# Kernel tuning notes

Hardware: AMD Instinct MI355X
Metric: run time of the kernel (lower is better)

Reference implementation:

```python
import jax, jax.numpy as jnp
import numpy as np

N = 50000
D = 128
E = 600000

def setup_inputs() -> dict:
    key = jax.random.key(0)
    k1, k2, k3, k4, k5 = jax.random.split(key, 5)
    z1 = jax.random.normal(k1, (N, D), dtype=jnp.float32)
    z2 = jax.random.normal(k2, (N, D), dtype=jnp.float32)
    adj_row = jax.random.randint(k3, (E,), 0, N, dtype=jnp.int32)
    adj_col = jax.random.randint(k4, (E,), 0, N, dtype=jnp.int32)
    adj_val = jax.random.uniform(k5, (E,), dtype=jnp.float32)
    a = jnp.full((N, D), 0.5, dtype=jnp.float32)
    b = jnp.full((N, D), 0.5, dtype=jnp.float32)
    alpha = jnp.float32(0.5)
    return {"z1": z1, "z2": z2, "adj_row": adj_row, "adj_col": adj_col,
            "adj_val": adj_val, "a": a, "b": b, "alpha": alpha}

def reference(z1, z2, adj_row, adj_col, adj_val, a, b, alpha):
    # elementwise gated combine: z_i = a*z1 + b*z2   [N, D]
    z_i = a * z1 + b * z2
    # sparse matmul: z_l[r] = sum_e adj_val[e] * z_i[adj_col[e]] for adj_row[e]==r
    msgs = adj_val[:, None] * z_i[adj_col]          # [E, D]
    z_l = jax.ops.segment_sum(msgs, adj_row, num_segments=N)  # [N, D]
    # residual blend
    return alpha * z_l + (1.0 - alpha) * z_i
```

## Files before the change

### kernel.cpp

```cpp
#include <hip/hip_runtime.h>
#include <hip/hip_fp16.h>

#define DDIM 128
#define CAPMAX 32

__global__ void __launch_bounds__(256) build_kernel(
    const float4* __restrict__ z1, const float4* __restrict__ z2,
    const float4* __restrict__ a,  const float4* __restrict__ b,
    uint2* __restrict__ zi16, int n4,
    const int* __restrict__ rows, const int* __restrict__ cols,
    const float* __restrict__ vals,
    unsigned* __restrict__ slots, int* __restrict__ cnt,
    int* __restrict__ ohead, int* __restrict__ onext,
    int cap, int E) {
  if (blockIdx.x & 1) {
    const int t = (int)(blockIdx.x >> 1) * blockDim.x + threadIdx.x;
    const int stride = (int)(gridDim.x >> 1) * blockDim.x;
    for (int e0 = t; e0 < E; e0 += 2 * stride) {
      const int e1 = e0 + stride;
      const bool has1 = e1 < E;
      const int   r0 = rows[e0];
      const int   c0 = cols[e0];
      const float v0 = vals[e0];
      const int   r1 = has1 ? rows[e1] : 0;
      const int   c1 = has1 ? cols[e1] : 0;
      const float v1 = has1 ? vals[e1] : 0.f;
      const int j0 = atomicAdd(&cnt[r0], 1);
      const int j1 = has1 ? atomicAdd(&cnt[r1], 1) : 0;
      if (j0 < cap) {
        const unsigned hv = (unsigned)__half_as_ushort(__float2half_rn(v0));
        slots[(size_t)r0 * cap + j0] = (unsigned)c0 | (hv << 16);
      } else {
        onext[e0] = atomicExch(&ohead[r0], e0 + 1);
      }
      if (has1) {
        if (j1 < cap) {
          const unsigned hv = (unsigned)__half_as_ushort(__float2half_rn(v1));
          slots[(size_t)r1 * cap + j1] = (unsigned)c1 | (hv << 16);
        } else {
          onext[e1] = atomicExch(&ohead[r1], e1 + 1);
        }
      }
    }
  } else {
    const int t = (int)(blockIdx.x >> 1) * blockDim.x + threadIdx.x;
    const int stride = (int)(gridDim.x >> 1) * blockDim.x;
    for (int j = t; j < n4; j += stride) {
      float4 A = a[j], B = b[j], X = z1[j], Y = z2[j];
      __half2 h0 = __floats2half2_rn(A.x * X.x + B.x * Y.x,
                                     A.y * X.y + B.y * Y.y);
      __half2 h1 = __floats2half2_rn(A.z * X.z + B.z * Y.z,
                                     A.w * X.w + B.w * Y.w);
      uint2 pk;
      pk.x = *reinterpret_cast<unsigned*>(&h0);
      pk.y = *reinterpret_cast<unsigned*>(&h1);
      zi16[j] = pk;
    }
  }
}

__global__ void __launch_bounds__(256) reduce_kernel(
    const unsigned* __restrict__ slots, const int* __restrict__ cnt,
    const int* __restrict__ ohead, const int* __restrict__ onext,
    const int* __restrict__ cols, const float* __restrict__ vals,
    const float* __restrict__ alpha_p,
    const __half2* __restrict__ zi16, float2* __restrict__ out2,
    int cap, int N) {
  const int r = (int)((blockIdx.x * blockDim.x + threadIdx.x) >> 6);
  const int lane = threadIdx.x & 63;
  if (r >= N) return;
  const float alpha = alpha_p[0];

  const __half2 zr16 = zi16[(size_t)r * (DDIM / 2) + lane];

  const int deg = cnt[r];
  const int m = deg < cap ? deg : cap;
  const unsigned* sp = slots + (size_t)r * cap;
  const uint4* sp4 = (const uint4*)sp;

  float2 a0 = make_float2(0.f, 0.f), a1 = a0, a2 = a0, a3 = a0;
  float2 a4 = a0, a5 = a0, a6 = a0, a7 = a0;
  int j = 0;
  for (; j + 8 <= m; j += 8) {
    const uint4 p0 = sp4[(j >> 2) + 0];
    const uint4 p1 = sp4[(j >> 2) + 1];
    const __half2 g0 = zi16[(size_t)(p0.x & 0xFFFF) * (DDIM / 2) + lane];
    const __half2 g1 = zi16[(size_t)(p0.y & 0xFFFF) * (DDIM / 2) + lane];
    const __half2 g2 = zi16[(size_t)(p0.z & 0xFFFF) * (DDIM / 2) + lane];
    const __half2 g3 = zi16[(size_t)(p0.w & 0xFFFF) * (DDIM / 2) + lane];
    const __half2 g4 = zi16[(size_t)(p1.x & 0xFFFF) * (DDIM / 2) + lane];
    const __half2 g5 = zi16[(size_t)(p1.y & 0xFFFF) * (DDIM / 2) + lane];
    const __half2 g6 = zi16[(size_t)(p1.z & 0xFFFF) * (DDIM / 2) + lane];
    const __half2 g7 = zi16[(size_t)(p1.w & 0xFFFF) * (DDIM / 2) + lane];
    const float2 f0 = __half22float2(g0), f1 = __half22float2(g1);
    const float2 f2 = __half22float2(g2), f3 = __half22float2(g3);
    const float2 f4 = __half22float2(g4), f5 = __half22float2(g5);
    const float2 f6 = __half22float2(g6), f7 = __half22float2(g7);
    const float v0 = __half2float(__ushort_as_half((unsigned short)(p0.x >> 16)));
    const float v1 = __half2float(__ushort_as_half((unsigned short)(p0.y >> 16)));
    const float v2 = __half2float(__ushort_as_half((unsigned short)(p0.z >> 16)));
    const float v3 = __half2float(__ushort_as_half((unsigned short)(p0.w >> 16)));
    const float v4 = __half2float(__ushort_as_half((unsigned short)(p1.x >> 16)));
    const float v5 = __half2float(__ushort_as_half((unsigned short)(p1.y >> 16)));
    const float v6 = __half2float(__ushort_as_half((unsigned short)(p1.z >> 16)));
    const float v7 = __half2float(__ushort_as_half((unsigned short)(p1.w >> 16)));
    a0.x += v0 * f0.x; a0.y += v0 * f0.y;
    a1.x += v1 * f1.x; a1.y += v1 * f1.y;
    a2.x += v2 * f2.x; a2.y += v2 * f2.y;
    a3.x += v3 * f3.x; a3.y += v3 * f3.y;
    a4.x += v4 * f4.x; a4.y += v4 * f4.y;
    a5.x += v5 * f5.x; a5.y += v5 * f5.y;
    a6.x += v6 * f6.x; a6.y += v6 * f6.y;
    a7.x += v7 * f7.x; a7.y += v7 * f7.y;
  }
  for (; j < m; ++j) {
    const unsigned s = sp[j];
    const float v = __half2float(__ushort_as_half((unsigned short)(s >> 16)));
    const float2 f =
        __half22float2(zi16[(size_t)(s & 0xFFFF) * (DDIM / 2) + lane]);
    a0.x += v * f.x; a0.y += v * f.y;
  }
  if (deg > cap) {
    int e1 = ohead[r];
    while (e1 > 0) {
      const int e = e1 - 1;
      e1 = onext[e];
      const int c = cols[e];
      const float v = vals[e];
      const float2 f = __half22float2(zi16[(size_t)c * (DDIM / 2) + lane]);
      a0.x += v * f.x; a0.y += v * f.y;
    }
  }

  float2 acc;
  acc.x = ((a0.x + a1.x) + (a2.x + a3.x)) + ((a4.x + a5.x) + (a6.x + a7.x));
  acc.y = ((a0.y + a1.y) + (a2.y + a3.y)) + ((a4.y + a5.y) + (a6.y + a7.y));
  const float2 zr = __half22float2(zr16);
  const float om = 1.0f - alpha;
  float2 o;
  o.x = alpha * acc.x + om * zr.x;
  o.y = alpha * acc.y + om * zr.y;
  out2[(size_t)r * (DDIM / 2) + lane] = o;
}

extern "C" void kernel_launch(void* const* d_in, const int* in_sizes, int n_in,
                              void* d_out, int out_size, void* d_ws, size_t ws_size,
                              hipStream_t stream) {
  const float* z1    = (const float*)d_in[0];
  const float* z2    = (const float*)d_in[1];
  const int*   rows  = (const int*)  d_in[2];
  const int*   cols  = (const int*)  d_in[3];
  const float* vals  = (const float*)d_in[4];
  const float* a     = (const float*)d_in[5];
  const float* b     = (const float*)d_in[6];
  const float* alpha = (const float*)d_in[7];
  float* out = (float*)d_out;

  const int ND = in_sizes[0];
  const int E  = in_sizes[2];
  const int N  = ND / DDIM;
  const int n4 = ND / 4;

  __half2* zi16 = (__half2*)d_ws;
  int* cnt   = (int*)((char*)d_ws + (size_t)ND * 2);
  int* ohead = cnt + N;
  int* onext = ohead + N;
  unsigned* slots = (unsigned*)(onext + E);

  const size_t fixed_bytes = (size_t)ND * 2 + ((size_t)2 * N + E) * 4;
  size_t avail = ws_size > fixed_bytes ? ws_size - fixed_bytes : 0;
  int cap = (int)(avail / ((size_t)N * sizeof(unsigned)));
  if (cap > CAPMAX) cap = CAPMAX;
  cap &= ~3;
  if (cap < 4) cap = 0;

  hipMemsetAsync(cnt, 0x00, (size_t)2 * N * sizeof(int), stream);

  build_kernel<<<2048, 256, 0, stream>>>(
      (const float4*)z1, (const float4*)z2, (const float4*)a,
      (const float4*)b, (uint2*)zi16, n4,
      rows, cols, vals, slots, cnt, ohead, onext, cap, E);

  const int blocks2 = (int)(((long long)N * 64 + 255) / 256);
  reduce_kernel<<<blocks2, 256, 0, stream>>>(
      slots, cnt, ohead, onext, cols, vals, alpha,
      zi16, (float2*)out, cap, N);
}
```

Measured before the change: 192.0 us.

## Split edge bucketing into eight per-partition slot arrays with separate counters

Edge bucketing now uses eight partitions, chosen by block index. Each partition has its own per-row counters and slot arrays, aiming to spread atomic contention on the row counters. The build kernel no longer splits blocks between the combine and the bucketing; every thread does the fp16 combine first and then processes edges. The reduce kernel reads all eight partition counters and the first uint4 of each partition's slots, then runs unrolled predicated gathers. In exchange it adds counter and slot traffic, a larger memset, and extra branching per row, when the average degree is already small.

```diff
diff --git a/kernel.cpp b/kernel.cpp
--- a/kernel.cpp
+++ b/kernel.cpp
@@ -2,7 +2,8 @@
 #include <hip/hip_fp16.h>
 
 #define DDIM 128
-#define CAPMAX 32
+#define NPART 8
+#define CAP8MAX 16
 
 __global__ void __launch_bounds__(256) build_kernel(
     const float4* __restrict__ z1, const float4* __restrict__ z2,
@@ -10,62 +11,62 @@
     uint2* __restrict__ zi16, int n4,
     const int* __restrict__ rows, const int* __restrict__ cols,
     const float* __restrict__ vals,
-    unsigned* __restrict__ slots, int* __restrict__ cnt,
+    unsigned* __restrict__ slots, int* __restrict__ cnt8,
     int* __restrict__ ohead, int* __restrict__ onext,
-    int cap, int E) {
-  if (blockIdx.x & 1) {
-    const int t = (int)(blockIdx.x >> 1) * blockDim.x + threadIdx.x;
-    const int stride = (int)(gridDim.x >> 1) * blockDim.x;
-    for (int e0 = t; e0 < E; e0 += 2 * stride) {
-      const int e1 = e0 + stride;
-      const bool has1 = e1 < E;
-      const int   r0 = rows[e0];
-      const int   c0 = cols[e0];
-      const float v0 = vals[e0];
-      const int   r1 = has1 ? rows[e1] : 0;
-      const int   c1 = has1 ? cols[e1] : 0;
-      const float v1 = has1 ? vals[e1] : 0.f;
-      const int j0 = atomicAdd(&cnt[r0], 1);
-      const int j1 = has1 ? atomicAdd(&cnt[r1], 1) : 0;
-      if (j0 < cap) {
-        const unsigned hv = (unsigned)__half_as_ushort(__float2half_rn(v0));
-        slots[(size_t)r0 * cap + j0] = (unsigned)c0 | (hv << 16);
+    int cap8, int N, int E) {
+  const int t = (int)blockIdx.x * (int)blockDim.x + threadIdx.x;
+  const int stride = (int)gridDim.x * (int)blockDim.x;
+
+  for (int j = t; j < n4; j += stride) {
+    float4 A = a[j], B = b[j], X = z1[j], Y = z2[j];
+    __half2 h0 = __floats2half2_rn(A.x * X.x + B.x * Y.x,
+                                   A.y * X.y + B.y * Y.y);
+    __half2 h1 = __floats2half2_rn(A.z * X.z + B.z * Y.z,
+                                   A.w * X.w + B.w * Y.w);
+    uint2 pk;
+    pk.x = *reinterpret_cast<unsigned*>(&h0);
+    pk.y = *reinterpret_cast<unsigned*>(&h1);
+    zi16[j] = pk;
+  }
+
+  const int p = (int)blockIdx.x & (NPART - 1);
+  int* __restrict__ mycnt = cnt8 + (size_t)p * N;
+  unsigned* __restrict__ myslots = slots + (size_t)p * N * cap8;
+  for (int e0 = t; e0 < E; e0 += 2 * stride) {
+    const int e1 = e0 + stride;
+    const bool has1 = e1 < E;
+    const int   r0 = rows[e0];
+    const int   c0 = cols[e0];
+    const float v0 = vals[e0];
+    const int   r1 = has1 ? rows[e1] : 0;
+    const int   c1 = has1 ? cols[e1] : 0;
+    const float v1 = has1 ? vals[e1] : 0.f;
+    const int j0 = atomicAdd(&mycnt[r0], 1);
+    const int j1 = has1 ? atomicAdd(&mycnt[r1], 1) : 0;
+    if (j0 < cap8) {
+      const unsigned hv = (unsigned)__half_as_ushort(__float2half_rn(v0));
+      myslots[(size_t)r0 * cap8 + j0] = (unsigned)c0 | (hv << 16);
+    } else {
+      onext[e0] = atomicExch(&ohead[r0], e0 + 1);
+    }
+    if (has1) {
+      if (j1 < cap8) {
+        const unsigned hv = (unsigned)__half_as_ushort(__float2half_rn(v1));
+        myslots[(size_t)r1 * cap8 + j1] = (unsigned)c1 | (hv << 16);
       } else {
-        onext[e0] = atomicExch(&ohead[r0], e0 + 1);
+        onext[e1] = atomicExch(&ohead[r1], e1 + 1);
       }
-      if (has1) {
-        if (j1 < cap) {
-          const unsigned hv = (unsigned)__half_as_ushort(__float2half_rn(v1));
-          slots[(size_t)r1 * cap + j1] = (unsigned)c1 | (hv << 16);
-        } else {
-          onext[e1] = atomicExch(&ohead[r1], e1 + 1);
-        }
-      }
-    }
-  } else {
-    const int t = (int)(blockIdx.x >> 1) * blockDim.x + threadIdx.x;
-    const int stride = (int)(gridDim.x >> 1) * blockDim.x;
-    for (int j = t; j < n4; j += stride) {
-      float4 A = a[j], B = b[j], X = z1[j], Y = z2[j];
-      __half2 h0 = __floats2half2_rn(A.x * X.x + B.x * Y.x,
-                                     A.y * X.y + B.y * Y.y);
-      __half2 h1 = __floats2half2_rn(A.z * X.z + B.z * Y.z,
-                                     A.w * X.w + B.w * Y.w);
-      uint2 pk;
-      pk.x = *reinterpret_cast<unsigned*>(&h0);
-      pk.y = *reinterpret_cast<unsigned*>(&h1);
-      zi16[j] = pk;
     }
   }
 }
 
 __global__ void __launch_bounds__(256) reduce_kernel(
-    const unsigned* __restrict__ slots, const int* __restrict__ cnt,
+    const unsigned* __restrict__ slots, const int* __restrict__ cnt8,
     const int* __restrict__ ohead, const int* __restrict__ onext,
     const int* __restrict__ cols, const float* __restrict__ vals,
     const float* __restrict__ alpha_p,
     const __half2* __restrict__ zi16, float2* __restrict__ out2,
-    int cap, int N) {
+    int cap8, int N) {
   const int r = (int)((blockIdx.x * blockDim.x + threadIdx.x) >> 6);
   const int lane = threadIdx.x & 63;
   if (r >= N) return;
@@ -73,68 +74,54 @@
 
   const __half2 zr16 = zi16[(size_t)r * (DDIM / 2) + lane];
 
-  const int deg = cnt[r];
-  const int m = deg < cap ? deg : cap;
-  const unsigned* sp = slots + (size_t)r * cap;
-  const uint4* sp4 = (const uint4*)sp;
+  int mp[NPART];
+  uint4 q[NPART];
+  bool over = false;
+#pragma unroll
+  for (int p = 0; p < NPART; ++p) {
+    const int dp = cnt8[(size_t)p * N + r];
+    mp[p] = dp < cap8 ? dp : cap8;
+    over = over || (dp > cap8);
+    q[p] = *(const uint4*)(slots + ((size_t)p * N + r) * cap8);
+  }
 
   float2 a0 = make_float2(0.f, 0.f), a1 = a0, a2 = a0, a3 = a0;
-  float2 a4 = a0, a5 = a0, a6 = a0, a7 = a0;
-  int j = 0;
-  for (; j + 8 <= m; j += 8) {
-    const uint4 p0 = sp4[(j >> 2) + 0];
-    const uint4 p1 = sp4[(j >> 2) + 1];
-    const __half2 g0 = zi16[(size_t)(p0.x & 0xFFFF) * (DDIM / 2) + lane];
-    const __half2 g1 = zi16[(size_t)(p0.y & 0xFFFF) * (DDIM / 2) + lane];
-    const __half2 g2 = zi16[(size_t)(p0.z & 0xFFFF) * (DDIM / 2) + lane];
-    const __half2 g3 = zi16[(size_t)(p0.w & 0xFFFF) * (DDIM / 2) + lane];
-    const __half2 g4 = zi16[(size_t)(p1.x & 0xFFFF) * (DDIM / 2) + lane];
-    const __half2 g5 = zi16[(size_t)(p1.y & 0xFFFF) * (DDIM / 2) + lane];
-    const __half2 g6 = zi16[(size_t)(p1.z & 0xFFFF) * (DDIM / 2) + lane];
-    const __half2 g7 = zi16[(size_t)(p1.w & 0xFFFF) * (DDIM / 2) + lane];
-    const float2 f0 = __half22float2(g0), f1 = __half22float2(g1);
-    const float2 f2 = __half22float2(g2), f3 = __half22float2(g3);
-    const float2 f4 = __half22float2(g4), f5 = __half22float2(g5);
-    const float2 f6 = __half22float2(g6), f7 = __half22float2(g7);
-    const float v0 = __half2float(__ushort_as_half((unsigned short)(p0.x >> 16)));
-    const float v1 = __half2float(__ushort_as_half((unsigned short)(p0.y >> 16)));
-    const float v2 = __half2float(__ushort_as_half((unsigned short)(p0.z >> 16)));
-    const float v3 = __half2float(__ushort_as_half((unsigned short)(p0.w >> 16)));
-    const float v4 = __half2float(__ushort_as_half((unsigned short)(p1.x >> 16)));
-    const float v5 = __half2float(__ushort_as_half((unsigned short)(p1.y >> 16)));
-    const float v6 = __half2float(__ushort_as_half((unsigned short)(p1.z >> 16)));
-    const float v7 = __half2float(__ushort_as_half((unsigned short)(p1.w >> 16)));
-    a0.x += v0 * f0.x; a0.y += v0 * f0.y;
-    a1.x += v1 * f1.x; a1.y += v1 * f1.y;
-    a2.x += v2 * f2.x; a2.y += v2 * f2.y;
-    a3.x += v3 * f3.x; a3.y += v3 * f3.y;
-    a4.x += v4 * f4.x; a4.y += v4 * f4.y;
-    a5.x += v5 * f5.x; a5.y += v5 * f5.y;
-    a6.x += v6 * f6.x; a6.y += v6 * f6.y;
-    a7.x += v7 * f7.x; a7.y += v7 * f7.y;
+#define EDGE(word, ACC)                                                       \
+  {                                                                           \
+    const unsigned s_ = (word);                                               \
+    const float v_ = __half2float(__ushort_as_half((unsigned short)(s_ >> 16)));\
+    const float2 f_ =                                                         \
+        __half22float2(zi16[(size_t)(s_ & 0xFFFF) * (DDIM / 2) + lane]);      \
+    ACC.x += v_ * f_.x;                                                       \
+    ACC.y += v_ * f_.y;                                                       \
   }
-  for (; j < m; ++j) {
-    const unsigned s = sp[j];
-    const float v = __half2float(__ushort_as_half((unsigned short)(s >> 16)));
-    const float2 f =
-        __half22float2(zi16[(size_t)(s & 0xFFFF) * (DDIM / 2) + lane]);
-    a0.x += v * f.x; a0.y += v * f.y;
+#pragma unroll
+  for (int p = 0; p < NPART; ++p) {
+    const int m = mp[p];
+    if (m > 0) EDGE(q[p].x, a0)
+    if (m > 1) EDGE(q[p].y, a1)
+    if (m > 2) EDGE(q[p].z, a2)
+    if (m > 3) EDGE(q[p].w, a3)
+    if (m > 4) {
+      const unsigned* sp = slots + ((size_t)p * N + r) * cap8;
+      for (int j = 4; j < m; ++j) EDGE(sp[j], a0)
+    }
   }
-  if (deg > cap) {
+  if (over) {
     int e1 = ohead[r];
     while (e1 > 0) {
       const int e = e1 - 1;
       e1 = onext[e];
-      const int c = cols[e];
       const float v = vals[e];
-      const float2 f = __half22float2(zi16[(size_t)c * (DDIM / 2) + lane]);
+      const float2 f = __half22float2(zi16[(size_t)cols[e] * (DDIM / 2) + lane]);
       a0.x += v * f.x; a0.y += v * f.y;
     }
   }
+#undef EDGE
 
   float2 acc;
-  acc.x = ((a0.x + a1.x) + (a2.x + a3.x)) + ((a4.x + a5.x) + (a6.x + a7.x));
-  acc.y = ((a0.y + a1.y) + (a2.y + a3.y)) + ((a4.y + a5.y) + (a6.y + a7.y));
+  acc.x = (a0.x + a1.x) + (a2.x + a3.x);
+  acc.y = (a0.y + a1.y) + (a2.y + a3.y);
   const float2 zr = __half22float2(zr16);
   const float om = 1.0f - alpha;
   float2 o;
@@ -162,27 +149,28 @@
   const int n4 = ND / 4;
 
   __half2* zi16 = (__half2*)d_ws;
-  int* cnt   = (int*)((char*)d_ws + (size_t)ND * 2);
-  int* ohead = cnt + N;
+  int* cnt8  = (int*)((char*)d_ws + (size_t)ND * 2);
+  int* ohead = cnt8 + (size_t)NPART * N;
   int* onext = ohead + N;
   unsigned* slots = (unsigned*)(onext + E);
 
-  const size_t fixed_bytes = (size_t)ND * 2 + ((size_t)2 * N + E) * 4;
+  const size_t fixed_bytes = (size_t)ND * 2 +
+                             ((size_t)NPART * N + N + E) * 4;
   size_t avail = ws_size > fixed_bytes ? ws_size - fixed_bytes : 0;
-  int cap = (int)(avail / ((size_t)N * sizeof(unsigned)));
-  if (cap > CAPMAX) cap = CAPMAX;
-  cap &= ~3;
-  if (cap < 4) cap = 0;
+  int cap8 = (int)(avail / ((size_t)NPART * N * sizeof(unsigned)));
+  if (cap8 > CAP8MAX) cap8 = CAP8MAX;
+  cap8 &= ~3;
+  if (cap8 < 4) cap8 = 0;
 
-  hipMemsetAsync(cnt, 0x00, (size_t)2 * N * sizeof(int), stream);
+  hipMemsetAsync(cnt8, 0x00, (size_t)(NPART + 1) * N * sizeof(int), stream);
 
   build_kernel<<<2048, 256, 0, stream>>>(
       (const float4*)z1, (const float4*)z2, (const float4*)a,
       (const float4*)b, (uint2*)zi16, n4,
-      rows, cols, vals, slots, cnt, ohead, onext, cap, E);
+      rows, cols, vals, slots, cnt8, ohead, onext, cap8, N, E);
 
   const int blocks2 = (int)(((long long)N * 64 + 255) / 256);
   reduce_kernel<<<blocks2, 256, 0, stream>>>(
-      slots, cnt, ohead, onext, cols, vals, alpha,
-      zi16, (float2*)out, cap, N);
+      slots, cnt8, ohead, onext, cols, vals, alpha,
+      zi16, (float2*)out, cap8, N);
 }
```

Measured after the change: 227.2 us. 1.18x slower.
